# Kernel optimization log

Hardware: AMD Instinct MI355X
Metric: run time of the kernel (lower is better)

## Reference

```python
import jax, jax.numpy as jnp
import numpy as np

RADIUS = 0.1
MAX_GRID_DIM = 96
MAX_COLLISIONS = 128


def setup_inputs() -> dict:
    key = jax.random.key(0)
    k1, k2 = jax.random.split(key)
    locs = jax.random.uniform(k1, (2, 4096, 3), dtype=jnp.float32)
    data = jax.random.normal(k2, (2, 4096, 16), dtype=jnp.float32)
    return {"locs": locs, "data": data}


def _cell_ids(locs):
    # Reproduces the grid-bound math in ParticleCollision.forward.
    lower = locs.min(axis=1)   # [B,D]
    upper = locs.max(axis=1)   # [B,D]
    grid_dims = jnp.ceil(jnp.clip((upper - lower) / RADIUS, 0.0, MAX_GRID_DIM))
    center = (lower + upper) * 0.5
    lower = center - grid_dims * RADIUS * 0.5
    gd = jnp.maximum(grid_dims, 1.0)
    cells = jnp.floor((locs - lower[:, None, :]) / RADIUS)
    cells = jnp.clip(cells, 0.0, gd[:, None, :] - 1.0).astype(jnp.int32)
    gdi = gd.astype(jnp.int32)  # [B,D]
    # Row-major strides per batch: stride[d] = prod(gdi[d+1:])
    rev_cp = jnp.cumprod(gdi[:, ::-1], axis=1)[:, ::-1]  # [B,D]
    strides = jnp.concatenate(
        [rev_cp[:, 1:], jnp.ones((gdi.shape[0], 1), jnp.int32)], axis=1)
    return (cells * strides[:, None, :]).sum(-1)  # [B,N]


def reference(locs, data):
    B, N, D = locs.shape
    cell_ids = _cell_ids(locs)
    # Stable sort by cell id (mirrors the radix sort); idxs = original index
    # of each particle in the new (sorted) order.
    order = jnp.argsort(cell_ids, axis=1, stable=True)  # [B,N]
    locs_s = jnp.take_along_axis(locs, order[:, :, None], axis=1)  # reordered locs
    data_s = jnp.take_along_axis(data, order[:, :, None], axis=1)  # reordered data
    # Pairwise squared distances without materializing [B,N,N,D].
    sq = (locs_s * locs_s).sum(-1)  # [B,N]
    d2 = sq[:, :, None] + sq[:, None, :] - 2.0 * jnp.einsum(
        'bnd,bmd->bnm', locs_s, locs_s)  # [B,N,N]
    mask = d2 <= RADIUS * RADIUS
    # First MAX_COLLISIONS in-radius neighbors per particle (ascending index
    # in sorted order), -1 padding past the end of each neighbor list.
    keys = jnp.where(mask, jnp.int32(0), jnp.int32(1))
    nbr = jnp.argsort(keys, axis=-1, stable=True)[:, :, :MAX_COLLISIONS]
    valid = jnp.take_along_axis(mask, nbr, axis=-1)
    neighbors = jnp.where(valid, nbr, -1).astype(jnp.float32)  # [B,N,M]
    idxs = order.astype(jnp.float32)  # [B,N]
    return idxs, neighbors, locs_s, data_s
```

## Files before the change

kernel.cpp:

```cpp
#include <hip/hip_runtime.h>

#define NPART 4096
#define NBATCH 2
#define MAXC 128

__global__ __launch_bounds__(256) void rank_kernel(
    const float* __restrict__ locs, unsigned short* __restrict__ partial,
    int njlog2, int jspan) {
  const int bx = blockIdx.x;
  const int tid = threadIdx.x;
  const int jslice = bx & ((1 << njlog2) - 1);
  const int ic = (bx >> njlog2) & 15;
  const int b = bx >> (njlog2 + 4);

  __shared__ float smn[3][256];
  __shared__ float smx[3][256];
  __shared__ int scj[256];
  __shared__ float sb_lower[3];
  __shared__ int sb_gdi[3];

  const float* base = locs + (size_t)b * NPART * 3;
  float mn0 = 1e30f, mn1 = 1e30f, mn2 = 1e30f;
  float mx0 = -1e30f, mx1 = -1e30f, mx2 = -1e30f;
  for (int n = tid; n < NPART; n += 256) {
    float x = base[n * 3 + 0];
    float y = base[n * 3 + 1];
    float z = base[n * 3 + 2];
    mn0 = fminf(mn0, x); mx0 = fmaxf(mx0, x);
    mn1 = fminf(mn1, y); mx1 = fmaxf(mx1, y);
    mn2 = fminf(mn2, z); mx2 = fmaxf(mx2, z);
  }
  smn[0][tid] = mn0; smn[1][tid] = mn1; smn[2][tid] = mn2;
  smx[0][tid] = mx0; smx[1][tid] = mx1; smx[2][tid] = mx2;
  __syncthreads();
  for (int s = 128; s > 0; s >>= 1) {
    if (tid < s) {
      for (int d = 0; d < 3; d++) {
        smn[d][tid] = fminf(smn[d][tid], smn[d][tid + s]);
        smx[d][tid] = fmaxf(smx[d][tid], smx[d][tid + s]);
      }
    }
    __syncthreads();
  }
  if (tid == 0) {
    for (int d = 0; d < 3; d++) {
      float lo = smn[d][0];
      float up = smx[d][0];
      float t = (up - lo) / 0.1f;
      t = fminf(fmaxf(t, 0.0f), 96.0f);
      float gdim = ceilf(t);
      float ctr = (lo + up) * 0.5f;
      float l2 = ctr - ((gdim * 0.1f) * 0.5f);
      float g = fmaxf(gdim, 1.0f);
      sb_lower[d] = l2;
      sb_gdi[d] = (int)g;
    }
  }
  __syncthreads();

  auto cid = [&](int n) {
    int c[3];
    for (int d = 0; d < 3; d++) {
      float v = base[n * 3 + d];
      float cf = floorf((v - sb_lower[d]) / 0.1f);
      float gdf = (float)sb_gdi[d];
      cf = fminf(fmaxf(cf, 0.0f), gdf - 1.0f);
      c[d] = (int)cf;
    }
    return (c[0] * sb_gdi[1] + c[1]) * sb_gdi[2] + c[2];
  };

  const int ci = cid(ic * 256 + tid);
  int cnt = 0;
  for (int jj = 0; jj < jspan; jj++) {
    int jc = jslice * jspan + jj;
    __syncthreads();
    scj[tid] = cid(jc * 256 + tid);
    __syncthreads();
    if (jc < ic) {
#pragma unroll 8
      for (int j = 0; j < 256; j++) cnt += (scj[j] <= ci);
    } else if (jc > ic) {
#pragma unroll 8
      for (int j = 0; j < 256; j++) cnt += (scj[j] < ci);
    } else {
#pragma unroll 8
      for (int j = 0; j < 256; j++) {
        int cj = scj[j];
        cnt += (cj < ci) || (cj == ci && j < tid);
      }
    }
  }
  partial[(size_t)jslice * (NBATCH * NPART) + b * NPART + ic * 256 + tid] =
      (unsigned short)cnt;
}

__global__ __launch_bounds__(256) void scatgather_kernel(
    const float* __restrict__ locs, const float* __restrict__ data,
    const unsigned short* __restrict__ partial, int nj,
    float* __restrict__ out_idxs, float* __restrict__ out_locs,
    float* __restrict__ out_data, float4* __restrict__ slocs) {
  int p = blockIdx.x * 256 + threadIdx.x;
  int pb = p >> 12;
  int i = p & (NPART - 1);
  int r = 0;
  for (int s = 0; s < nj; s++)
    r += (int)partial[(size_t)s * (NBATCH * NPART) + p];
  const float* src = locs + (size_t)p * 3;
  float x = src[0], y = src[1], z = src[2];
  float sq = __fadd_rn(__fadd_rn(__fmul_rn(x, x), __fmul_rn(y, y)),
                       __fmul_rn(z, z));
  size_t dst = (size_t)pb * NPART + r;
  out_idxs[dst] = (float)i;
  out_locs[dst * 3 + 0] = x;
  out_locs[dst * 3 + 1] = y;
  out_locs[dst * 3 + 2] = z;
  slocs[dst] = make_float4(x, y, z, sq);
  const float4* dsrc = (const float4*)(data + (size_t)p * 16);
  float4* ddst = (float4*)(out_data + dst * 16);
  for (int k = 0; k < 4; k++) ddst[k] = dsrc[k];
}

__global__ __launch_bounds__(256) void nbr_kernel(
    const float4* __restrict__ slocs, float* __restrict__ out_nbr) {
  const int b = blockIdx.y;
  __shared__ float4 sl[2048];
  const int tid = threadIdx.x;
  const int wave = tid >> 6, lane = tid & 63;
  const int row0 = blockIdx.x * 8 + wave * 2;
  const float4* sb = slocs + (size_t)b * NPART;
  const float4 me0 = sb[row0 + 0];
  const float4 me1 = sb[row0 + 1];
  float* r0 = out_nbr + ((size_t)b * NPART + row0) * MAXC;
  float* r1 = r0 + MAXC;
  int c0 = 0, c1 = 0;
  const unsigned long long lmask = (1ull << lane) - 1ull;
  for (int half = 0; half < 2; half++) {
    const int hbase = half * 2048;
    __syncthreads();
    for (int k = 0; k < 8; k++) {
      int j = k * 256 + tid;
      __builtin_amdgcn_global_load_lds(
          (const __attribute__((address_space(1))) unsigned int*)(sb + hbase +
                                                                  j),
          (__attribute__((address_space(3))) unsigned int*)&sl[j], 16, 0, 0);
    }
    __syncthreads();
#pragma unroll 4
    for (int base = 0; base < 2048; base += 64) {
      float4 o = sl[base + lane];
      float fm = (float)(hbase + base + lane);
#define DO_ROW(ME, CN, RP)                                                  \
      {                                                                     \
        float dot = __fmaf_rn(ME.z, o.z,                                    \
                     __fmaf_rn(ME.y, o.y, __fmul_rn(ME.x, o.x)));           \
        float d2 = __fsub_rn(__fadd_rn(ME.w, o.w), __fmul_rn(2.0f, dot));   \
        bool hit = d2 <= 0.01f;                                             \
        unsigned long long bal = __ballot(hit);                             \
        int pos = CN + __popcll(bal & lmask);                               \
        if (hit && pos < MAXC) RP[pos] = fm;                                \
        CN += __popcll(bal);                                                \
      }
      DO_ROW(me0, c0, r0)
      DO_ROW(me1, c1, r1)
#undef DO_ROW
    }
  }
  for (int q = min(c0, MAXC) + lane; q < MAXC; q += 64) r0[q] = -1.0f;
  for (int q = min(c1, MAXC) + lane; q < MAXC; q += 64) r1[q] = -1.0f;
}

extern "C" void kernel_launch(void* const* d_in, const int* in_sizes, int n_in,
                              void* d_out, int out_size, void* d_ws,
                              size_t ws_size, hipStream_t stream) {
  const float* locs = (const float*)d_in[0];
  const float* data = (const float*)d_in[1];

  float* out = (float*)d_out;
  float* out_idxs = out;
  float* out_nbr = out + NBATCH * NPART;
  float* out_locs = out_nbr + (size_t)NBATCH * NPART * MAXC;
  float* out_data = out_locs + (size_t)NBATCH * NPART * 3;

  float4* slocs = (float4*)d_ws;
  unsigned short* partial =
      (unsigned short*)((char*)d_ws + (size_t)NBATCH * NPART * 16);

  size_t base_bytes = (size_t)NBATCH * NPART * 16;
  int nj, njlog2;
  if (ws_size >= base_bytes + 16ull * NBATCH * NPART * 2) {
    nj = 16; njlog2 = 4;
  } else {
    nj = 4; njlog2 = 2;
  }
  int jspan = 16 / nj;

  rank_kernel<<<NBATCH * 16 * nj, 256, 0, stream>>>(locs, partial, njlog2,
                                                    jspan);
  scatgather_kernel<<<NBATCH * NPART / 256, 256, 0, stream>>>(
      locs, data, partial, nj, out_idxs, out_locs, out_data, slocs);
  nbr_kernel<<<dim3(NPART / 8, NBATCH), 256, 0, stream>>>(slocs, out_nbr);
}
```

Baseline: 91.00 us.

## Reuse neighbor output buffer for rank partials and drop float4 sorted-locs workspace

```diff
diff --git a/kernel.cpp b/kernel.cpp
--- a/kernel.cpp
+++ b/kernel.cpp
@@ -5,13 +5,12 @@
 #define MAXC 128
 
 __global__ __launch_bounds__(256) void rank_kernel(
-    const float* __restrict__ locs, unsigned short* __restrict__ partial,
-    int njlog2, int jspan) {
+    const float* __restrict__ locs, unsigned short* __restrict__ partial) {
   const int bx = blockIdx.x;
   const int tid = threadIdx.x;
-  const int jslice = bx & ((1 << njlog2) - 1);
-  const int ic = (bx >> njlog2) & 15;
-  const int b = bx >> (njlog2 + 4);
+  const int jslice = bx & 15;
+  const int ic = (bx >> 4) & 15;
+  const int b = bx >> 8;
 
   __shared__ float smn[3][256];
   __shared__ float smx[3][256];
@@ -71,24 +70,22 @@
   };
 
   const int ci = cid(ic * 256 + tid);
+  const int jc = jslice;
+  scj[tid] = cid(jc * 256 + tid);
+  __syncthreads();
+
   int cnt = 0;
-  for (int jj = 0; jj < jspan; jj++) {
-    int jc = jslice * jspan + jj;
-    __syncthreads();
-    scj[tid] = cid(jc * 256 + tid);
-    __syncthreads();
-    if (jc < ic) {
+  if (jc < ic) {
 #pragma unroll 8
-      for (int j = 0; j < 256; j++) cnt += (scj[j] <= ci);
-    } else if (jc > ic) {
+    for (int j = 0; j < 256; j++) cnt += (scj[j] <= ci);
+  } else if (jc > ic) {
 #pragma unroll 8
-      for (int j = 0; j < 256; j++) cnt += (scj[j] < ci);
-    } else {
+    for (int j = 0; j < 256; j++) cnt += (scj[j] < ci);
+  } else {
 #pragma unroll 8
-      for (int j = 0; j < 256; j++) {
-        int cj = scj[j];
-        cnt += (cj < ci) || (cj == ci && j < tid);
-      }
+    for (int j = 0; j < 256; j++) {
+      int cj = scj[j];
+      cnt += (cj < ci) || (cj == ci && j < tid);
     }
   }
   partial[(size_t)jslice * (NBATCH * NPART) + b * NPART + ic * 256 + tid] =
@@ -97,40 +94,52 @@
 
 __global__ __launch_bounds__(256) void scatgather_kernel(
     const float* __restrict__ locs, const float* __restrict__ data,
-    const unsigned short* __restrict__ partial, int nj,
-    float* __restrict__ out_idxs, float* __restrict__ out_locs,
-    float* __restrict__ out_data, float4* __restrict__ slocs) {
+    const unsigned short* __restrict__ partial, float* __restrict__ out_idxs,
+    float* __restrict__ out_locs, float* __restrict__ out_data) {
   int p = blockIdx.x * 256 + threadIdx.x;
   int pb = p >> 12;
   int i = p & (NPART - 1);
   int r = 0;
-  for (int s = 0; s < nj; s++)
+#pragma unroll
+  for (int s = 0; s < 16; s++)
     r += (int)partial[(size_t)s * (NBATCH * NPART) + p];
   const float* src = locs + (size_t)p * 3;
   float x = src[0], y = src[1], z = src[2];
-  float sq = __fadd_rn(__fadd_rn(__fmul_rn(x, x), __fmul_rn(y, y)),
-                       __fmul_rn(z, z));
   size_t dst = (size_t)pb * NPART + r;
   out_idxs[dst] = (float)i;
   out_locs[dst * 3 + 0] = x;
   out_locs[dst * 3 + 1] = y;
   out_locs[dst * 3 + 2] = z;
-  slocs[dst] = make_float4(x, y, z, sq);
   const float4* dsrc = (const float4*)(data + (size_t)p * 16);
   float4* ddst = (float4*)(out_data + dst * 16);
   for (int k = 0; k < 4; k++) ddst[k] = dsrc[k];
 }
 
 __global__ __launch_bounds__(256) void nbr_kernel(
-    const float4* __restrict__ slocs, float* __restrict__ out_nbr) {
+    const float* __restrict__ slocs, float* __restrict__ out_nbr) {
   const int b = blockIdx.y;
   __shared__ float4 sl[2048];
   const int tid = threadIdx.x;
   const int wave = tid >> 6, lane = tid & 63;
   const int row0 = blockIdx.x * 8 + wave * 2;
-  const float4* sb = slocs + (size_t)b * NPART;
-  const float4 me0 = sb[row0 + 0];
-  const float4 me1 = sb[row0 + 1];
+  const float* sb = slocs + (size_t)b * NPART * 3;
+
+  float4 me0, me1;
+  {
+    float x = sb[(size_t)row0 * 3 + 0];
+    float y = sb[(size_t)row0 * 3 + 1];
+    float z = sb[(size_t)row0 * 3 + 2];
+    float w = __fadd_rn(__fadd_rn(__fmul_rn(x, x), __fmul_rn(y, y)),
+                        __fmul_rn(z, z));
+    me0 = make_float4(x, y, z, w);
+    x = sb[(size_t)(row0 + 1) * 3 + 0];
+    y = sb[(size_t)(row0 + 1) * 3 + 1];
+    z = sb[(size_t)(row0 + 1) * 3 + 2];
+    w = __fadd_rn(__fadd_rn(__fmul_rn(x, x), __fmul_rn(y, y)),
+                  __fmul_rn(z, z));
+    me1 = make_float4(x, y, z, w);
+  }
+
   float* r0 = out_nbr + ((size_t)b * NPART + row0) * MAXC;
   float* r1 = r0 + MAXC;
   int c0 = 0, c1 = 0;
@@ -138,12 +147,14 @@
   for (int half = 0; half < 2; half++) {
     const int hbase = half * 2048;
     __syncthreads();
+#pragma unroll
     for (int k = 0; k < 8; k++) {
       int j = k * 256 + tid;
-      __builtin_amdgcn_global_load_lds(
-          (const __attribute__((address_space(1))) unsigned int*)(sb + hbase +
-                                                                  j),
-          (__attribute__((address_space(3))) unsigned int*)&sl[j], 16, 0, 0);
+      const float* sp = sb + (size_t)(hbase + j) * 3;
+      float x = sp[0], y = sp[1], z = sp[2];
+      float w = __fadd_rn(__fadd_rn(__fmul_rn(x, x), __fmul_rn(y, y)),
+                          __fmul_rn(z, z));
+      sl[j] = make_float4(x, y, z, w);
     }
     __syncthreads();
 #pragma unroll 4
@@ -182,22 +193,12 @@
   float* out_locs = out_nbr + (size_t)NBATCH * NPART * MAXC;
   float* out_data = out_locs + (size_t)NBATCH * NPART * 3;
 
-  float4* slocs = (float4*)d_ws;
-  unsigned short* partial =
-      (unsigned short*)((char*)d_ws + (size_t)NBATCH * NPART * 16);
-
-  size_t base_bytes = (size_t)NBATCH * NPART * 16;
-  int nj, njlog2;
-  if (ws_size >= base_bytes + 16ull * NBATCH * NPART * 2) {
-    nj = 16; njlog2 = 4;
-  } else {
-    nj = 4; njlog2 = 2;
-  }
-  int jspan = 16 / nj;
-
-  rank_kernel<<<NBATCH * 16 * nj, 256, 0, stream>>>(locs, partial, njlog2,
-                                                    jspan);
+  unsigned short* partial = (unsigned short*)out_nbr;
+
+  (void)d_ws; (void)ws_size;
+
+  rank_kernel<<<NBATCH * 16 * 16, 256, 0, stream>>>(locs, partial);
   scatgather_kernel<<<NBATCH * NPART / 256, 256, 0, stream>>>(
-      locs, data, partial, nj, out_idxs, out_locs, out_data, slocs);
-  nbr_kernel<<<dim3(NPART / 8, NBATCH), 256, 0, stream>>>(slocs, out_nbr);
-}
+      locs, data, partial, out_idxs, out_locs, out_data);
+  nbr_kernel<<<dim3(NPART / 8, NBATCH), 256, 0, stream>>>(out_locs, out_nbr);
+}
```

After: 88.86 us. 2.4% less time.
